# Kernel optimization log

Hardware: AMD Instinct MI355X
Metric: run time of the kernel (lower is better)

## Reference

```python
import jax, jax.numpy as jnp
import numpy as np

N_NODES = 100000
N_EDGES = 1600000
NFEAT = 256
NHID = 128
NCLASS = 8


def setup_inputs() -> dict:
    key = jax.random.key(0)
    k1, k2, k3, k4, k5 = jax.random.split(key, 5)
    x = jax.random.normal(k1, (N_NODES, NFEAT), dtype=jnp.float32)
    edge_index = jax.random.randint(k2, (2, N_EDGES), 0, N_NODES, dtype=jnp.int64)
    # GCNConv weight (glorot) and bias
    s1 = float(np.sqrt(6.0 / (NFEAT + NHID)))
    W1 = jax.random.uniform(k3, (NFEAT, NHID), dtype=jnp.float32, minval=-s1, maxval=s1)
    b1 = jnp.zeros((NHID,), dtype=jnp.float32)
    # fc Linear (xavier uniform per weights_init, bias zero)
    s2 = float(np.sqrt(6.0 / (NHID + NCLASS)))
    Wfc = jax.random.uniform(k4, (NHID, NCLASS), dtype=jnp.float32, minval=-s2, maxval=s2)
    bfc = jnp.zeros((NCLASS,), dtype=jnp.float32)
    return {"x": x, "edge_index": edge_index, "W1": W1, "b1": b1, "Wfc": Wfc, "bfc": bfc}


def gcn_conv(x, src, dst, W, b, n_nodes):
    # PyG GCNConv: h = X W; out_i = sum_j norm_ij * h_j over A+I with sym norm
    h = x @ W  # [N, nhid]
    deg = jax.ops.segment_sum(jnp.ones_like(dst, dtype=h.dtype), dst, num_segments=n_nodes)
    dinv = jnp.where(deg > 0, jax.lax.rsqrt(deg), 0.0)  # deg^{-1/2}
    norm = dinv[src] * dinv[dst]  # [E+N]
    msg = h[src] * norm[:, None]  # gather + scale, [E+N, nhid]
    out = jax.ops.segment_sum(msg, dst, num_segments=n_nodes)
    return out + b


def reference(x, edge_index, W1, b1, Wfc, bfc):
    n = x.shape[0]
    loop = jnp.arange(n, dtype=edge_index.dtype)
    src = jnp.concatenate([edge_index[0], loop])  # add self-loops
    dst = jnp.concatenate([edge_index[1], loop])
    h = gcn_conv(x, src, dst, W1, b1, n)  # GCN_Body (no activation in forward)
    return h @ Wfc + bfc  # fc
```

## Files before the change

kernel.cpp:

```cpp
#include <hip/hip_runtime.h>
#include <hip/hip_bf16.h>

#define N_NODES 100000
#define N_EDGES 1600000
#define NFEAT 256
#define NHID 128
#define NCLASS 8

#define NBLK 512
#define BSH 9
#define NBUCK ((N_NODES + 511) >> 9)

__global__ __launch_bounds__(256) void hist_kernel(const int* __restrict__ edst,
                                                   int* __restrict__ blockhist,
                                                   int chunk, int nE) {
    __shared__ int h[NBUCK];
    int tid = threadIdx.x;
    for (int i = tid; i < NBUCK; i += 256) h[i] = 0;
    __syncthreads();
    int e0 = blockIdx.x * chunk;
    int e1 = min(e0 + chunk, nE);
    for (int e = e0 + tid; e < e1; e += 256)
        atomicAdd(&h[edst[e] >> BSH], 1);
    __syncthreads();
    for (int i = tid; i < NBUCK; i += 256)
        blockhist[(long)blockIdx.x * NBUCK + i] = h[i];
}

__global__ __launch_bounds__(256) void scanblk_kernel(const int* __restrict__ blockhist,
                                                      int* __restrict__ blockbase,
                                                      int* __restrict__ bucket_total) {
    __shared__ int ss[256];
    int b = blockIdx.x, tid = threadIdx.x;
    int v0 = blockhist[(long)tid * NBUCK + b];
    int v1 = blockhist[(long)(tid + 256) * NBUCK + b];
    int t = v0 + v1;
    ss[tid] = t; __syncthreads();
    for (int o = 1; o < 256; o <<= 1) {
        int u = (tid >= o) ? ss[tid - o] : 0;
        __syncthreads(); ss[tid] += u; __syncthreads();
    }
    int ex = ss[tid] - t;
    blockbase[(long)tid * NBUCK + b] = ex;
    blockbase[(long)(tid + 256) * NBUCK + b] = ex + v0;
    if (tid == 255) bucket_total[b] = ss[255];
}

__global__ __launch_bounds__(256) void scanbuck_kernel(const int* __restrict__ bucket_total,
                                                       int* __restrict__ bucket_base,
                                                       int* __restrict__ rowptr) {
    __shared__ int ss[256];
    int tid = threadIdx.x;
    int v = (tid < NBUCK) ? bucket_total[tid] : 0;
    ss[tid] = v; __syncthreads();
    for (int o = 1; o < 256; o <<= 1) {
        int u = (tid >= o) ? ss[tid - o] : 0;
        __syncthreads(); ss[tid] += u; __syncthreads();
    }
    if (tid < NBUCK) bucket_base[tid] = ss[tid] - v;
    if (tid == NBUCK - 1) { bucket_base[NBUCK] = ss[tid]; rowptr[N_NODES] = ss[tid]; }
}

__global__ __launch_bounds__(256) void scat_kernel(const int* __restrict__ esrc,
                                                   const int* __restrict__ edst,
                                                   const int* __restrict__ blockbase,
                                                   const int* __restrict__ bucket_base,
                                                   int2* __restrict__ ebuf2,
                                                   int chunk, int nE) {
    __shared__ int cur[NBUCK];
    int tid = threadIdx.x;
    for (int i = tid; i < NBUCK; i += 256)
        cur[i] = bucket_base[i] + blockbase[(long)blockIdx.x * NBUCK + i];
    __syncthreads();
    int e0 = blockIdx.x * chunk;
    int e1 = min(e0 + chunk, nE);
    for (int e = e0 + tid; e < e1; e += 256) {
        int s = esrc[e];
        int d = edst[e];
        int pos = atomicAdd(&cur[d >> BSH], 1);
        ebuf2[pos] = make_int2(s, d);
    }
}

__global__ __launch_bounds__(256) void build_kernel(const int2* __restrict__ ebuf2,
                                                    const int* __restrict__ bucket_base,
                                                    int* __restrict__ rowptr,
                                                    float* __restrict__ dinv,
                                                    int* __restrict__ ebuf) {
    __shared__ int cnt[512];
    __shared__ int off[512];
    __shared__ int ss[256];
    int b = blockIdx.x, tid = threadIdx.x;
    int base = bucket_base[b], end = bucket_base[b + 1];

    for (int i = tid; i < 512; i += 256) cnt[i] = 0;
    __syncthreads();
    for (int e = base + tid; e < end; e += 256)
        atomicAdd(&cnt[ebuf2[e].y & 511], 1);
    __syncthreads();

    int c0 = cnt[2 * tid], c1 = cnt[2 * tid + 1];
    int t = c0 + c1;
    ss[tid] = t; __syncthreads();
    for (int o = 1; o < 256; o <<= 1) {
        int u = (tid >= o) ? ss[tid - o] : 0;
        __syncthreads(); ss[tid] += u; __syncthreads();
    }
    int ex = ss[tid] - t;
    off[2 * tid] = ex; off[2 * tid + 1] = ex + c0;
    __syncthreads();

    int node0 = b << BSH;
    for (int i = tid; i < 512; i += 256) {
        int node = node0 + i;
        if (node < N_NODES) {
            rowptr[node] = base + off[i];
            dinv[node]   = rsqrtf((float)(cnt[i] + 1));
        }
    }
    for (int i = tid; i < 512; i += 256) cnt[i] = 0;
    __syncthreads();
    for (int e = base + tid; e < end; e += 256) {
        int2 sd = ebuf2[e];
        int li = sd.y & 511;
        int r = atomicAdd(&cnt[li], 1);
        ebuf[base + off[li] + r] = sd.x;
    }
}

__global__ __launch_bounds__(256) void wc_kernel(const float* __restrict__ W1,
                                                 const float* __restrict__ b1,
                                                 const float* __restrict__ Wfc,
                                                 const float* __restrict__ bfc,
                                                 float* __restrict__ WcT,
                                                 float* __restrict__ cvec) {
    __shared__ float wfs[NHID * NCLASS];
    __shared__ float bs[NHID];
    int tid = threadIdx.x;
    for (int i = tid; i < NHID * NCLASS; i += 256) wfs[i] = Wfc[i];
    if (tid < NHID) bs[tid] = b1[tid];
    __syncthreads();

    float acc[NCLASS] = {};
    for (int h = 0; h < NHID; h++) {
        float w = W1[tid * NHID + h];
        #pragma unroll
        for (int c = 0; c < NCLASS; c++) acc[c] += w * wfs[h * NCLASS + c];
    }
    #pragma unroll
    for (int c = 0; c < NCLASS; c++) WcT[c * NFEAT + tid] = acc[c];

    if (tid < NCLASS) {
        float a = bfc[tid];
        for (int h = 0; h < NHID; h++) a += bs[h] * wfs[h * NCLASS + tid];
        cvec[tid] = a;
    }
}

__global__ __launch_bounds__(256) void z_kernel(const float* __restrict__ X,
                                                const float* __restrict__ WcT,
                                                const float* __restrict__ dinv,
                                                float* __restrict__ Zs, int n) {
    __shared__ float4 wlds[NCLASS * 64];
    int tid = threadIdx.x;
    #pragma unroll
    for (int i = tid; i < NCLASS * 64; i += 256)
        wlds[i] = ((const float4*)WcT)[i];
    __syncthreads();

    const int lane = tid & 63;
    const int sub  = lane & 7;
    const int rsub = lane >> 3;
    const int wid  = (blockIdx.x * 256 + tid) >> 6;
    const int nw   = (gridDim.x * 256) >> 6;
    const int ngroups = (n + 7) >> 3;

    for (int g = wid; g < ngroups; g += nw) {
        int row = g * 8 + rsub;
        bool ok = row < n;
        int r = ok ? row : (n - 1);
        const float4* xr = (const float4*)(X + (long)r * NFEAT);
        float4 xv[8];
        #pragma unroll
        for (int k = 0; k < 8; k++) xv[k] = xr[sub + 8 * k];

        float res = 0.f;
        #pragma unroll
        for (int c = 0; c < NCLASS; c++) {
            float s = 0.f;
            #pragma unroll
            for (int k = 0; k < 8; k++) {
                float4 w = wlds[c * 64 + sub + 8 * k];
                s += xv[k].x * w.x + xv[k].y * w.y + xv[k].z * w.z + xv[k].w * w.w;
            }
            s += __shfl_xor(s, 1);
            s += __shfl_xor(s, 2);
            s += __shfl_xor(s, 4);
            if (sub == c) res = s;
        }
        if (ok) Zs[(long)row * NCLASS + sub] = res * dinv[row];
    }
}

__global__ __launch_bounds__(256) void gather_fc_kernel(const float* __restrict__ Zs,
                                                        const int* __restrict__ ebuf,
                                                        const int* __restrict__ rowptr,
                                                        const float* __restrict__ dinv,
                                                        const float* __restrict__ cvec,
                                                        float* __restrict__ out, int n) {
    int idx = blockIdx.x * 256 + threadIdx.x;
    if (idx >= 2 * n) return;
    int node = idx >> 1;
    int h    = idx & 1;
    int s0 = rowptr[node], s1 = rowptr[node + 1];
    const float4* Zs4 = (const float4*)Zs;

    float4 a = Zs4[node * 2 + h];
    int k = s0;
    for (; k + 1 < s1; k += 2) {
        int i0 = ebuf[k], i1 = ebuf[k + 1];
        float4 z0 = Zs4[i0 * 2 + h];
        float4 z1 = Zs4[i1 * 2 + h];
        a.x += z0.x + z1.x; a.y += z0.y + z1.y;
        a.z += z0.z + z1.z; a.w += z0.w + z1.w;
    }
    if (k < s1) {
        float4 z = Zs4[ebuf[k] * 2 + h];
        a.x += z.x; a.y += z.y; a.z += z.z; a.w += z.w;
    }

    float dd = dinv[node];
    float4 cv = ((const float4*)cvec)[h];
    float4 o;
    o.x = a.x * dd + cv.x; o.y = a.y * dd + cv.y;
    o.z = a.z * dd + cv.z; o.w = a.w * dd + cv.w;
    ((float4*)out)[node * 2 + h] = o;
}

extern "C" void kernel_launch(void* const* d_in, const int* in_sizes, int n_in,
                              void* d_out, int out_size, void* d_ws, size_t ws_size,
                              hipStream_t stream) {
    const float* x    = (const float*)d_in[0];
    const int*   eidx = (const int*)d_in[1];
    const float* W1   = (const float*)d_in[2];
    const float* b1   = (const float*)d_in[3];
    const float* Wfc  = (const float*)d_in[4];
    const float* bfc  = (const float*)d_in[5];
    float* out = (float*)d_out;

    const int N = N_NODES;
    const int E = in_sizes[1] / 2;
    const int chunk = (E + NBLK - 1) / NBLK;

    const int* esrc = eidx;
    const int* edst = eidx + E;

    float* Zs     = (float*)d_ws;
    float* dinv   = Zs + (long)8 * N;
    int*   rowptr = (int*)(dinv + N);
    float* cvec   = (float*)(rowptr + N + 4);
    float* WcT    = cvec + 8;
    int*   btot   = (int*)(WcT + NCLASS * NFEAT);
    int*   bbase  = btot + NBUCK;
    int*   bhist  = bbase + NBUCK + 4;
    int*   bbas2  = bhist + NBLK * NBUCK;
    size_t ofs = (size_t)(bbas2 + NBLK * NBUCK - (int*)d_ws);
    ofs = (ofs + 3) & ~(size_t)3;
    int2*  ebuf2  = (int2*)((int*)d_ws + ofs);
    int*   ebuf   = (int*)(ebuf2 + E);

    wc_kernel<<<1, 256, 0, stream>>>(W1, b1, Wfc, bfc, WcT, cvec);

    hist_kernel<<<NBLK, 256, 0, stream>>>(edst, bhist, chunk, E);
    scanblk_kernel<<<NBUCK, 256, 0, stream>>>(bhist, bbas2, btot);
    scanbuck_kernel<<<1, 256, 0, stream>>>(btot, bbase, rowptr);
    scat_kernel<<<NBLK, 256, 0, stream>>>(esrc, edst, bbas2, bbase, ebuf2, chunk, E);
    build_kernel<<<NBUCK, 256, 0, stream>>>(ebuf2, bbase, rowptr, dinv, ebuf);

    z_kernel<<<1563, 256, 0, stream>>>(x, WcT, dinv, Zs, N);

    gather_fc_kernel<<<(2 * N + 255) / 256, 256, 0, stream>>>(
        Zs, ebuf, rowptr, dinv, cvec, out, N);
}
```

Baseline: 260.9 us.

## Replace CSR build with bucketed packed edges and LDS atomic aggregation

Drops the per-node CSR construction: edges are now only bucket-sorted by destination, with source and local destination packed into one int. Degrees come from a small per-bucket LDS histogram, and the final gather runs one block per 256-node bucket, accumulating messages with LDS float atomics before applying the norm and bias. The scan and weight-fold kernels are merged into one launch. This removes a second full edge pass, the rowptr and ebuf writes, and one launch, at the cost of heavy shared-memory atomics and a non-deterministic summation order. Packing assumes src<<8 fits in an int, which holds for 100k nodes.

Measured after the change: 315.1 us. 1.21x slower.

```diff
diff --git a/kernel.cpp b/kernel.cpp
--- a/kernel.cpp
+++ b/kernel.cpp
@@ -8,8 +8,9 @@
 #define NCLASS 8
 
 #define NBLK 512
-#define BSH 9
-#define NBUCK ((N_NODES + 511) >> 9)
+#define BSH 8
+#define BUCK 256
+#define NBUCK ((N_NODES + BUCK - 1) / BUCK)
 
 __global__ __launch_bounds__(256) void hist_kernel(const int* __restrict__ edst,
                                                    int* __restrict__ blockhist,
@@ -46,26 +47,54 @@
     if (tid == 255) bucket_total[b] = ss[255];
 }
 
-__global__ __launch_bounds__(256) void scanbuck_kernel(const int* __restrict__ bucket_total,
-                                                       int* __restrict__ bucket_base,
-                                                       int* __restrict__ rowptr) {
-    __shared__ int ss[256];
-    int tid = threadIdx.x;
-    int v = (tid < NBUCK) ? bucket_total[tid] : 0;
-    ss[tid] = v; __syncthreads();
-    for (int o = 1; o < 256; o <<= 1) {
-        int u = (tid >= o) ? ss[tid - o] : 0;
-        __syncthreads(); ss[tid] += u; __syncthreads();
-    }
-    if (tid < NBUCK) bucket_base[tid] = ss[tid] - v;
-    if (tid == NBUCK - 1) { bucket_base[NBUCK] = ss[tid]; rowptr[N_NODES] = ss[tid]; }
+__global__ __launch_bounds__(512) void mid_kernel(const int* __restrict__ bucket_total,
+                                                  int* __restrict__ bucket_base,
+                                                  const float* __restrict__ W1,
+                                                  const float* __restrict__ b1,
+                                                  const float* __restrict__ Wfc,
+                                                  const float* __restrict__ bfc,
+                                                  float* __restrict__ WcT,
+                                                  float* __restrict__ cvec) {
+    int tid = threadIdx.x;
+    if (blockIdx.x == 0) {
+        __shared__ int ss[512];
+        int v = (tid < NBUCK) ? bucket_total[tid] : 0;
+        ss[tid] = v; __syncthreads();
+        for (int o = 1; o < 512; o <<= 1) {
+            int u = (tid >= o) ? ss[tid - o] : 0;
+            __syncthreads(); ss[tid] += u; __syncthreads();
+        }
+        if (tid < NBUCK) bucket_base[tid] = ss[tid] - v;
+        if (tid == NBUCK - 1) bucket_base[NBUCK] = ss[tid];
+    } else {
+        __shared__ float wfs[NHID * NCLASS];
+        __shared__ float bs[NHID];
+        for (int i = tid; i < NHID * NCLASS; i += 512) wfs[i] = Wfc[i];
+        if (tid < NHID) bs[tid] = b1[tid];
+        __syncthreads();
+        if (tid < NFEAT) {
+            float acc[NCLASS] = {};
+            for (int h = 0; h < NHID; h++) {
+                float w = W1[tid * NHID + h];
+                #pragma unroll
+                for (int c = 0; c < NCLASS; c++) acc[c] += w * wfs[h * NCLASS + c];
+            }
+            #pragma unroll
+            for (int c = 0; c < NCLASS; c++) WcT[c * NFEAT + tid] = acc[c];
+        }
+        if (tid < NCLASS) {
+            float a = bfc[tid];
+            for (int h = 0; h < NHID; h++) a += bs[h] * wfs[h * NCLASS + tid];
+            cvec[tid] = a;
+        }
+    }
 }
 
 __global__ __launch_bounds__(256) void scat_kernel(const int* __restrict__ esrc,
                                                    const int* __restrict__ edst,
                                                    const int* __restrict__ blockbase,
                                                    const int* __restrict__ bucket_base,
-                                                   int2* __restrict__ ebuf2,
+                                                   int* __restrict__ ebufP,
                                                    int chunk, int nE) {
     __shared__ int cur[NBUCK];
     int tid = threadIdx.x;
@@ -78,83 +107,23 @@
         int s = esrc[e];
         int d = edst[e];
         int pos = atomicAdd(&cur[d >> BSH], 1);
-        ebuf2[pos] = make_int2(s, d);
-    }
-}
-
-__global__ __launch_bounds__(256) void build_kernel(const int2* __restrict__ ebuf2,
-                                                    const int* __restrict__ bucket_base,
-                                                    int* __restrict__ rowptr,
-                                                    float* __restrict__ dinv,
-                                                    int* __restrict__ ebuf) {
-    __shared__ int cnt[512];
-    __shared__ int off[512];
-    __shared__ int ss[256];
+        ebufP[pos] = (s << BSH) | (d & (BUCK - 1));
+    }
+}
+
+__global__ __launch_bounds__(256) void deg_dinv_kernel(const int* __restrict__ ebufP,
+                                                       const int* __restrict__ bucket_base,
+                                                       float* __restrict__ dinv) {
+    __shared__ int cnt[BUCK];
     int b = blockIdx.x, tid = threadIdx.x;
+    cnt[tid] = 0;
+    __syncthreads();
     int base = bucket_base[b], end = bucket_base[b + 1];
-
-    for (int i = tid; i < 512; i += 256) cnt[i] = 0;
-    __syncthreads();
     for (int e = base + tid; e < end; e += 256)
-        atomicAdd(&cnt[ebuf2[e].y & 511], 1);
-    __syncthreads();
-
-    int c0 = cnt[2 * tid], c1 = cnt[2 * tid + 1];
-    int t = c0 + c1;
-    ss[tid] = t; __syncthreads();
-    for (int o = 1; o < 256; o <<= 1) {
-        int u = (tid >= o) ? ss[tid - o] : 0;
-        __syncthreads(); ss[tid] += u; __syncthreads();
-    }
-    int ex = ss[tid] - t;
-    off[2 * tid] = ex; off[2 * tid + 1] = ex + c0;
-    __syncthreads();
-
-    int node0 = b << BSH;
-    for (int i = tid; i < 512; i += 256) {
-        int node = node0 + i;
-        if (node < N_NODES) {
-            rowptr[node] = base + off[i];
-            dinv[node]   = rsqrtf((float)(cnt[i] + 1));
-        }
-    }
-    for (int i = tid; i < 512; i += 256) cnt[i] = 0;
-    __syncthreads();
-    for (int e = base + tid; e < end; e += 256) {
-        int2 sd = ebuf2[e];
-        int li = sd.y & 511;
-        int r = atomicAdd(&cnt[li], 1);
-        ebuf[base + off[li] + r] = sd.x;
-    }
-}
-
-__global__ __launch_bounds__(256) void wc_kernel(const float* __restrict__ W1,
-                                                 const float* __restrict__ b1,
-                                                 const float* __restrict__ Wfc,
-                                                 const float* __restrict__ bfc,
-                                                 float* __restrict__ WcT,
-                                                 float* __restrict__ cvec) {
-    __shared__ float wfs[NHID * NCLASS];
-    __shared__ float bs[NHID];
-    int tid = threadIdx.x;
-    for (int i = tid; i < NHID * NCLASS; i += 256) wfs[i] = Wfc[i];
-    if (tid < NHID) bs[tid] = b1[tid];
-    __syncthreads();
-
-    float acc[NCLASS] = {};
-    for (int h = 0; h < NHID; h++) {
-        float w = W1[tid * NHID + h];
-        #pragma unroll
-        for (int c = 0; c < NCLASS; c++) acc[c] += w * wfs[h * NCLASS + c];
-    }
-    #pragma unroll
-    for (int c = 0; c < NCLASS; c++) WcT[c * NFEAT + tid] = acc[c];
-
-    if (tid < NCLASS) {
-        float a = bfc[tid];
-        for (int h = 0; h < NHID; h++) a += bs[h] * wfs[h * NCLASS + tid];
-        cvec[tid] = a;
-    }
+        atomicAdd(&cnt[ebufP[e] & (BUCK - 1)], 1);
+    __syncthreads();
+    int node = (b << BSH) + tid;
+    if (node < N_NODES) dinv[node] = rsqrtf((float)(cnt[tid] + 1));
 }
 
 __global__ __launch_bounds__(256) void z_kernel(const float* __restrict__ X,
@@ -202,39 +171,59 @@
     }
 }
 
-__global__ __launch_bounds__(256) void gather_fc_kernel(const float* __restrict__ Zs,
-                                                        const int* __restrict__ ebuf,
-                                                        const int* __restrict__ rowptr,
-                                                        const float* __restrict__ dinv,
-                                                        const float* __restrict__ cvec,
-                                                        float* __restrict__ out, int n) {
-    int idx = blockIdx.x * 256 + threadIdx.x;
-    if (idx >= 2 * n) return;
-    int node = idx >> 1;
-    int h    = idx & 1;
-    int s0 = rowptr[node], s1 = rowptr[node + 1];
+__global__ __launch_bounds__(512) void bucket_gather_kernel(
+        const float* __restrict__ Zs,
+        const int* __restrict__ ebufP,
+        const int* __restrict__ bucket_base,
+        const float* __restrict__ dinv,
+        const float* __restrict__ cvec,
+        float* __restrict__ out, int n) {
+    __shared__ float acc[NCLASS * BUCK];
+    int b = blockIdx.x, tid = threadIdx.x;
+    for (int i = tid; i < NCLASS * BUCK; i += 512) acc[i] = 0.f;
+    __syncthreads();
+
+    int base = bucket_base[b], end = bucket_base[b + 1];
     const float4* Zs4 = (const float4*)Zs;
 
-    float4 a = Zs4[node * 2 + h];
-    int k = s0;
-    for (; k + 1 < s1; k += 2) {
-        int i0 = ebuf[k], i1 = ebuf[k + 1];
-        float4 z0 = Zs4[i0 * 2 + h];
-        float4 z1 = Zs4[i1 * 2 + h];
-        a.x += z0.x + z1.x; a.y += z0.y + z1.y;
-        a.z += z0.z + z1.z; a.w += z0.w + z1.w;
-    }
-    if (k < s1) {
-        float4 z = Zs4[ebuf[k] * 2 + h];
-        a.x += z.x; a.y += z.y; a.z += z.z; a.w += z.w;
-    }
-
-    float dd = dinv[node];
-    float4 cv = ((const float4*)cvec)[h];
-    float4 o;
-    o.x = a.x * dd + cv.x; o.y = a.y * dd + cv.y;
-    o.z = a.z * dd + cv.z; o.w = a.w * dd + cv.w;
-    ((float4*)out)[node * 2 + h] = o;
+    for (int e = base + tid; e < end; e += 512) {
+        int p   = ebufP[e];
+        int src = p >> BSH;
+        int li  = p & (BUCK - 1);
+        float4 z0 = Zs4[src * 2];
+        float4 z1 = Zs4[src * 2 + 1];
+        atomicAdd(&acc[0 * BUCK + li], z0.x);
+        atomicAdd(&acc[1 * BUCK + li], z0.y);
+        atomicAdd(&acc[2 * BUCK + li], z0.z);
+        atomicAdd(&acc[3 * BUCK + li], z0.w);
+        atomicAdd(&acc[4 * BUCK + li], z1.x);
+        atomicAdd(&acc[5 * BUCK + li], z1.y);
+        atomicAdd(&acc[6 * BUCK + li], z1.z);
+        atomicAdd(&acc[7 * BUCK + li], z1.w);
+    }
+    __syncthreads();
+
+    if (tid < BUCK) {
+        int node = (b << BSH) + tid;
+        if (node < n) {
+            float4 s0 = Zs4[node * 2];
+            float4 s1 = Zs4[node * 2 + 1];
+            float dd = dinv[node];
+            float4 c0 = ((const float4*)cvec)[0];
+            float4 c1 = ((const float4*)cvec)[1];
+            float4 o0, o1;
+            o0.x = (s0.x + acc[0 * BUCK + tid]) * dd + c0.x;
+            o0.y = (s0.y + acc[1 * BUCK + tid]) * dd + c0.y;
+            o0.z = (s0.z + acc[2 * BUCK + tid]) * dd + c0.z;
+            o0.w = (s0.w + acc[3 * BUCK + tid]) * dd + c0.w;
+            o1.x = (s1.x + acc[4 * BUCK + tid]) * dd + c1.x;
+            o1.y = (s1.y + acc[5 * BUCK + tid]) * dd + c1.y;
+            o1.z = (s1.z + acc[6 * BUCK + tid]) * dd + c1.z;
+            o1.w = (s1.w + acc[7 * BUCK + tid]) * dd + c1.w;
+            ((float4*)out)[node * 2]     = o0;
+            ((float4*)out)[node * 2 + 1] = o1;
+        }
+    }
 }
 
 extern "C" void kernel_launch(void* const* d_in, const int* in_sizes, int n_in,
@@ -255,30 +244,21 @@
     const int* esrc = eidx;
     const int* edst = eidx + E;
 
-    float* Zs     = (float*)d_ws;
-    float* dinv   = Zs + (long)8 * N;
-    int*   rowptr = (int*)(dinv + N);
-    float* cvec   = (float*)(rowptr + N + 4);
-    float* WcT    = cvec + 8;
-    int*   btot   = (int*)(WcT + NCLASS * NFEAT);
-    int*   bbase  = btot + NBUCK;
-    int*   bhist  = bbase + NBUCK + 4;
-    int*   bbas2  = bhist + NBLK * NBUCK;
-    size_t ofs = (size_t)(bbas2 + NBLK * NBUCK - (int*)d_ws);
-    ofs = (ofs + 3) & ~(size_t)3;
-    int2*  ebuf2  = (int2*)((int*)d_ws + ofs);
-    int*   ebuf   = (int*)(ebuf2 + E);
-
-    wc_kernel<<<1, 256, 0, stream>>>(W1, b1, Wfc, bfc, WcT, cvec);
+    float* Zs    = (float*)d_ws;
+    float* dinv  = Zs + (long)8 * N;
+    float* cvec  = dinv + N;
+    float* WcT   = cvec + 8;
+    int*   btot  = (int*)(WcT + NCLASS * NFEAT);
+    int*   bbase = btot + NBUCK + 1;
+    int*   bhist = bbase + NBUCK + 3;
+    int*   bbas2 = bhist + (long)NBLK * NBUCK;
+    int*   ebufP = bbas2 + (long)NBLK * NBUCK;
 
     hist_kernel<<<NBLK, 256, 0, stream>>>(edst, bhist, chunk, E);
     scanblk_kernel<<<NBUCK, 256, 0, stream>>>(bhist, bbas2, btot);
-    scanbuck_kernel<<<1, 256, 0, stream>>>(btot, bbase, rowptr);
-    scat_kernel<<<NBLK, 256, 0, stream>>>(esrc, edst, bbas2, bbase, ebuf2, chunk, E);
-    build_kernel<<<NBUCK, 256, 0, stream>>>(ebuf2, bbase, rowptr, dinv, ebuf);
-
+    mid_kernel<<<2, 512, 0, stream>>>(btot, bbase, W1, b1, Wfc, bfc, WcT, cvec);
+    scat_kernel<<<NBLK, 256, 0, stream>>>(esrc, edst, bbas2, bbase, ebufP, chunk, E);
+    deg_dinv_kernel<<<NBUCK, 256, 0, stream>>>(ebufP, bbase, dinv);
     z_kernel<<<1563, 256, 0, stream>>>(x, WcT, dinv, Zs, N);
-
-    gather_fc_kernel<<<(2 * N + 255) / 256, 256, 0, stream>>>(
-        Zs, ebuf, rowptr, dinv, cvec, out, N);
-}
+    bucket_gather_kernel<<<NBUCK, 512, 0, stream>>>(Zs, ebufP, bbase, dinv, cvec, out, N);
+}
```
